# Kernel tuning notes

Measured on AMD Instinct MI355X. Metric: run time of the kernel, lower is better.

## Reference

```python
import jax, jax.numpy as jnp
import numpy as np

B, N, SD = 2, 128, 3
IN, H, BD, O, L, WF = 16, 128, 32, 12, 2, 4
DEGREE = 2
EPS = 1e-6


def fibonacci_lattice(n, offset=0.5):
    i = jnp.arange(n, dtype=jnp.float32)
    theta = (jnp.pi * i * (1.0 + np.sqrt(5.0))) % (2.0 * jnp.pi)
    phi = jnp.arccos(1.0 - 2.0 * (i + offset) / (n - 1 + 2 * offset))
    return jnp.stack((jnp.sin(phi) * jnp.cos(theta),
                      jnp.sin(phi) * jnp.sin(theta),
                      jnp.cos(phi)), axis=-1)  # (O, 3)


def poly_features(x, degree=DEGREE):
    feats = [x]
    for _ in range(degree):
        new = jnp.einsum('...i,...j->...ij', feats[-1], x).reshape(x.shape[:-1] + (-1,))
        feats.append(new)
    return jnp.concatenate(feats, axis=-1)


def layernorm(x, scale, bias):
    m = x.mean(axis=-1, keepdims=True)
    v = ((x - m) ** 2).mean(axis=-1, keepdims=True)
    return (x - m) * jax.lax.rsqrt(v + EPS) * scale + bias


def _dense(k, fin, fout):
    return jax.random.normal(k, (fin, fout), jnp.float32) / np.sqrt(fin)


def setup_inputs() -> dict:
    key = jax.random.key(0)
    ks = jax.random.split(key, 32)
    SP_IN = 2 + 4 + 8   # poly features of 2-dim spatial invariants, degree 2
    RO_IN = 1 + 1 + 1   # poly features of 1-dim orientation invariant
    inp = {
        'pos': jax.random.normal(ks[0], (B, N, SD), jnp.float32),
        'x': jax.random.normal(ks[1], (B, N, IN), jnp.float32),
        'mask': jnp.ones((B, N), jnp.float32),
        # spatial kernel basis MLP
        'W1s': _dense(ks[2], SP_IN, H), 'b1s': jnp.zeros((H,), jnp.float32),
        'W2s': _dense(ks[3], H, BD),    'b2s': jnp.zeros((BD,), jnp.float32),
        # rotation kernel basis MLP
        'W1r': _dense(ks[4], RO_IN, H), 'b1r': jnp.zeros((H,), jnp.float32),
        'W2r': _dense(ks[5], H, BD),    'b2r': jnp.zeros((BD,), jnp.float32),
        # x embedder (no bias)
        'We': _dense(ks[6], IN, H),
        # per-layer params, stacked along leading layer axis L
        'Wsp':  jax.random.normal(ks[7], (L, BD, H), jnp.float32) / np.sqrt(BD),
        'Wrot': jax.random.normal(ks[8], (L, BD, H), jnp.float32) / np.sqrt(BD),
        'conv_b': jnp.zeros((L, H), jnp.float32),
        'ln_scale': jnp.ones((L, H), jnp.float32),
        'ln_bias': jnp.zeros((L, H), jnp.float32),
        'Wl1': jax.random.normal(ks[9], (L, H, WF * H), jnp.float32) / np.sqrt(H),
        'bl1': jnp.zeros((L, WF * H), jnp.float32),
        'Wl2': jax.random.normal(ks[10], (L, WF * H, H), jnp.float32) / np.sqrt(WF * H),
        'bl2': jnp.zeros((L, H), jnp.float32),
        # readout
        'Wro': _dense(ks[11], H, 1), 'bro': jnp.zeros((1,), jnp.float32),
    }
    return inp


def reference(pos, x, mask, W1s, b1s, W2s, b2s, W1r, b1r, W2r, b2r, We,
              Wsp, Wrot, conv_b, ln_scale, ln_bias, Wl1, bl1, Wl2, bl2, Wro, bro):
    ori = fibonacci_lattice(O)                                   # (O, 3)
    # pairwise relative positions: (B, N_dst=m? note: original indexing)
    rel_pos = pos[:, None, :, None, :] - pos[:, :, None, None, :]  # (B,N,N,1,3)
    inv1 = (rel_pos * ori[None, None, None, :, :]).sum(-1, keepdims=True)        # (B,N,N,O,1)
    inv2 = jnp.linalg.norm(rel_pos - rel_pos * inv1, axis=-1, keepdims=True)     # (B,N,N,O,1)
    spatial_inv = jnp.concatenate([inv1, inv2], axis=-1)          # (B,N,N,O,2)
    ori_inv = (ori[:, None, :] * ori[None, :, :]).sum(-1, keepdims=True)         # (O,O,1)

    gelu = jax.nn.gelu  # approximate tanh gelu, matching flax nn.gelu default
    kernel_basis = gelu(gelu(poly_features(spatial_inv) @ W1s + b1s) @ W2s + b2s)   # (B,N,N,O,BD)
    fiber_basis = gelu(gelu(poly_features(ori_inv) @ W1r + b1r) @ W2r + b2r)        # (O,O,BD)

    h = x @ We                                                    # (B,N,H)
    h = jnp.broadcast_to(h[:, :, None, :], (h.shape[0], h.shape[1], O, h.shape[2]))

    for i in range(L):
        inp = h
        spatial_kernel = kernel_basis @ Wsp[i]                    # (B,N,N,O,H)
        rot_kernel = fiber_basis @ Wrot[i]                        # (O,O,H)
        h = jnp.einsum('bnoc,bmnoc,bn->bmoc', h, spatial_kernel, mask)
        h = jnp.einsum('bmoc,poc->bmpc', h, rot_kernel) / rot_kernel.shape[-2]
        h = h + conv_b[i]
        h = layernorm(h, ln_scale[i], ln_bias[i])
        h = gelu(h @ Wl1[i] + bl1[i]) @ Wl2[i] + bl2[i]
        h = h + inp

    readout = h @ Wro + bro                                       # (B,N,O,1)
    out_scalar = readout.mean(axis=-2)                            # (B,N,1)
    out_scalar = jnp.sum(out_scalar * mask[:, :, None], axis=1) / jnp.sum(mask[:, :, None], axis=1)
    return out_scalar                                             # (B,1)
```

## Files before the change

### kernel.cpp

```cpp
#include <hip/hip_runtime.h>
#include <math.h>

#define NB 2
#define NN 128
#define NO 12
#define NIN 16
#define NH 128
#define NBD 32
#define NL 2
#define NHH 512
#define NSPLIT 8

typedef __attribute__((ext_vector_type(8))) short bf16x8;
typedef __attribute__((ext_vector_type(4))) float f32x4;

__device__ __forceinline__ float gelu_f(float x){
    float x2 = x*x;
    float t = x*(2.3022077f + 0.1029435f*x2);
    float e = __builtin_amdgcn_exp2f(t);
    float r = __builtin_amdgcn_rcpf(e + 1.0f);
    return __builtin_fmaf(-x, r, x);
}

__device__ __forceinline__ ushort f2b(float x){
    union { float f; uint u; } v; v.f = x;
    uint r = v.u + 0x7FFF + ((v.u >> 16) & 1);
    return (ushort)(r >> 16);
}

#define MFMA_BF16(A,B,C) __builtin_amdgcn_mfma_f32_16x16x32_bf16(A,B,C,0,0,0)

__global__ __launch_bounds__(256) void k_setup(const float* __restrict__ W1r,
        const float* __restrict__ b1r, const float* __restrict__ W2r,
        const float* __restrict__ b2r, const float* __restrict__ W1s,
        const float* __restrict__ b1s, const float* __restrict__ W2s,
        float* __restrict__ ws_ori, float* __restrict__ ws_fiber,
        ushort* __restrict__ w1ct, ushort* __restrict__ w2ct){
    __shared__ float sori[NO*3];
    __shared__ float sb2r[NBD];
    __shared__ __align__(16) char sWT[8192];
    __shared__ __align__(16) char sHid[160*256];

    int tid = threadIdx.x;
    int w = tid >> 6, lane = tid & 63, lr = lane & 15, lg = lane >> 4;

    if (tid < NO){
        float fi = (float)tid;
        float th = fmodf(3.14159265358979323846f * fi * 3.23606797749979f,
                         6.28318530717958647692f);
        float ph = acosf(1.0f - 2.0f*(fi + 0.5f)/12.0f);
        float sp = sinf(ph);
        float ox = sp*cosf(th), oy = sp*sinf(th), oz = cosf(ph);
        sori[tid*3+0]=ox; sori[tid*3+1]=oy; sori[tid*3+2]=oz;
        ws_ori[tid*3+0]=ox; ws_ori[tid*3+1]=oy; ws_ori[tid*3+2]=oz;
    }
    if (tid < NBD) sb2r[tid] = b2r[tid];
    if (tid < NH){
        int c = tid;
        float r0 = b1s[c];
        float r1 = W1s[c], r2 = W1s[NH+c], r3 = W1s[2*NH+c];
        float r4 = W1s[3*NH+c] + W1s[4*NH+c];
        float r5 = W1s[5*NH+c], r6 = W1s[6*NH+c];
        float r7 = W1s[7*NH+c] + W1s[8*NH+c] + W1s[10*NH+c];
        float r8 = W1s[9*NH+c] + W1s[11*NH+c] + W1s[12*NH+c];
        float r9 = W1s[13*NH+c];
        ushort* p = w1ct + c*32;
        p[0]=f2b(r0); p[1]=f2b(r1); p[2]=f2b(r2); p[3]=f2b(r3); p[4]=f2b(r4);
        p[5]=f2b(r5); p[6]=f2b(r6); p[7]=f2b(r7); p[8]=f2b(r8); p[9]=f2b(r9);
        #pragma unroll
        for (int k = 10; k < 32; ++k) p[k] = 0;
    }
    for (int e = tid; e < NBD*NH; e += 256){
        int c = e >> 7, k = e & 127;
        w2ct[c*NH + k] = f2b(W2s[k*NBD + c]);
    }
    for (int e = tid; e < NBD*NH; e += 256){
        int c = e >> 7, k = e & 127;
        *(ushort*)(sWT + c*256 + ((k*2) ^ ((c & 7) << 4))) = f2b(W2r[k*NBD + c]);
    }
    for (int e = tid; e < 16*64; e += 256){
        int row = 144 + (e >> 6), k2 = e & 63;
        *(uint*)(sHid + row*256 + ((k2*4) ^ ((row & 7) << 4))) = 0u;
    }
    __syncthreads();
    for (int e = tid; e < 144*NH; e += 256){
        int t = e & 127, row = e >> 7;
        int p = row / NO, q = row - (row/NO)*NO;
        float xv = sori[p*3]*sori[q*3] + sori[p*3+1]*sori[q*3+1] + sori[p*3+2]*sori[q*3+2];
        float acc = b1r[t] + xv*(W1r[t] + xv*(W1r[NH+t] + xv*W1r[2*NH+t]));
        *(ushort*)(sHid + row*256 + ((t*2) ^ ((row & 7) << 4))) = f2b(gelu_f(acc));
    }
    __syncthreads();
    for (int tile = w; tile < 5; tile += 4){
        float bv0 = sb2r[lr], bv1 = sb2r[16 + lr];
        f32x4 acc2[2][2];
        acc2[0][0] = (f32x4){bv0,bv0,bv0,bv0}; acc2[0][1] = (f32x4){bv1,bv1,bv1,bv1};
        acc2[1][0] = acc2[0][0]; acc2[1][1] = acc2[0][1];
        #pragma unroll
        for (int kk = 0; kk < 4; ++kk){
            int kbyte = (kk*32 + lg*8)*2;
            int r0 = tile*32 + lr, r1 = r0 + 16;
            bf16x8 a0 = *(const bf16x8*)(sHid + r0*256 + (kbyte ^ ((r0 & 7) << 4)));
            bf16x8 a1 = *(const bf16x8*)(sHid + r1*256 + (kbyte ^ ((r1 & 7) << 4)));
            bf16x8 b0 = *(const bf16x8*)(sWT + lr*256 + (kbyte ^ ((lr & 7) << 4)));
            bf16x8 b1 = *(const bf16x8*)(sWT + (16+lr)*256 + (kbyte ^ ((lr & 7) << 4)));
            acc2[0][0] = MFMA_BF16(a0, b0, acc2[0][0]);
            acc2[0][1] = MFMA_BF16(a0, b1, acc2[0][1]);
            acc2[1][0] = MFMA_BF16(a1, b0, acc2[1][0]);
            acc2[1][1] = MFMA_BF16(a1, b1, acc2[1][1]);
        }
        #pragma unroll
        for (int i = 0; i < 2; ++i)
            #pragma unroll
            for (int j = 0; j < 2; ++j)
                #pragma unroll
                for (int r = 0; r < 4; ++r){
                    int row = tile*32 + i*16 + lg*4 + r, d = j*16 + lr;
                    if (row < 144) ws_fiber[row*NBD + d] = gelu_f(acc2[i][j][r]);
                }
    }
}

__global__ __launch_bounds__(256) void k_rot(const float* __restrict__ fiber,
        const float* __restrict__ Wrot, float* __restrict__ rot){
    int g = blockIdx.x*256 + threadIdx.x;
    int c = g & 127; int rest = g >> 7;
    int o = rest % NO; rest /= NO;
    int p = rest % NO; int i = rest / NO;
    const float* f = fiber + (p*NO + o)*NBD;
    const float* w = Wrot + (size_t)i*NBD*NH + c;
    float acc = 0.f;
    #pragma unroll
    for (int d = 0; d < NBD; ++d) acc += f[d]*w[d*NH];
    rot[g] = acc;
}

__global__ __launch_bounds__(256) void k_embed(const float* __restrict__ x,
        const float* __restrict__ We, float* __restrict__ hE){
    int g = blockIdx.x*256 + threadIdx.x;
    int c = g & 127; int n = (g >> 7) & 127; int b = g >> 14;
    const float* xp = x + ((size_t)b*NN + n)*NIN;
    float acc = 0.f;
    #pragma unroll
    for (int k = 0; k < NIN; ++k) acc += xp[k]*We[k*NH + c];
    hE[g] = acc;
}

__global__ __launch_bounds__(256) void k_kb(const float* __restrict__ pos,
        const ushort* __restrict__ w1ct, const ushort* __restrict__ w2ct,
        const float* __restrict__ b2s, const float* __restrict__ ori,
        ushort* __restrict__ kb){
    __shared__ __align__(16) char smem[49152];
    ushort* sF  = (ushort*)smem;
    char*  sWT  = smem + 8192;
    char*  sH   = smem + 16384;

    int tid = threadIdx.x;
    int bid = blockIdx.x;
    int m = bid & 127; int t2 = bid >> 7;
    int o = t2 % NO, b = t2 / NO;
    int w = tid >> 6, lane = tid & 63, lr = lane & 15, lg = lane >> 4;

    {
        const uint* src = (const uint*)w1ct;
        for (int e = tid; e < 2048; e += 256){
            int c = e >> 4, kk = e & 15;
            *(uint*)(sWT + c*64 + ((kk*4) ^ ((c & 3) << 4))) = src[e];
        }
    }
    if (tid < NN){
        int n = tid;
        float rx = pos[((size_t)b*NN+n)*3+0] - pos[((size_t)b*NN+m)*3+0];
        float ry = pos[((size_t)b*NN+n)*3+1] - pos[((size_t)b*NN+m)*3+1];
        float rz = pos[((size_t)b*NN+n)*3+2] - pos[((size_t)b*NN+m)*3+2];
        float ox = ori[o*3+0], oy = ori[o*3+1], oz = ori[o*3+2];
        float a  = rx*ox + ry*oy + rz*oz;
        float bb = sqrtf(rx*rx+ry*ry+rz*rz) * fabsf(1.0f - a);
        float a2 = a*a, b2 = bb*bb, ab = a*bb;
        float fv[10] = {1.0f, a, bb, a2, ab, b2, a2*a, a2*bb, a*b2, b2*bb};
        char* rowp = (char*)sF + n*64;
        int sw = (n & 3) << 4;
        #pragma unroll
        for (int kk = 0; kk < 5; ++kk){
            uint pk = (uint)f2b(fv[kk*2]) | ((uint)f2b(fv[kk*2+1]) << 16);
            *(uint*)(rowp + ((kk*4) ^ sw)) = pk;
        }
        #pragma unroll
        for (int kk = 5; kk < 16; ++kk)
            *(uint*)(rowp + ((kk*4) ^ sw)) = 0u;
    }
    __syncthreads();
    f32x4 hacc[2][8];
    {
        int rA0 = w*32 + lr, rA1 = rA0 + 16;
        bf16x8 fa0 = *(const bf16x8*)((char*)sF + rA0*64 + ((lg*16) ^ ((rA0 & 3) << 4)));
        bf16x8 fa1 = *(const bf16x8*)((char*)sF + rA1*64 + ((lg*16) ^ ((rA1 & 3) << 4)));
        #pragma unroll
        for (int j = 0; j < 8; ++j){
            int cB = j*16 + lr;
            bf16x8 fb = *(const bf16x8*)(sWT + cB*64 + ((lg*16) ^ ((cB & 3) << 4)));
            f32x4 z = (f32x4){0.f,0.f,0.f,0.f};
            hacc[0][j] = MFMA_BF16(fa0, fb, z);
            hacc[1][j] = MFMA_BF16(fa1, fb, z);
        }
    }
    #pragma unroll
    for (int i = 0; i < 2; ++i)
        #pragma unroll
        for (int j = 0; j < 8; ++j)
            #pragma unroll
            for (int r = 0; r < 4; ++r){
                int n = w*32 + i*16 + lg*4 + r;
                int c = j*16 + lr;
                *(ushort*)(sH + n*256 + ((c*2) ^ ((n & 7) << 4))) = f2b(gelu_f(hacc[i][j][r]));
            }
    __syncthreads();
    {
        const uint* src = (const uint*)w2ct;
        for (int e = tid; e < 2048; e += 256){
            int c = e >> 6, kk = e & 63;
            *(uint*)(sWT + c*256 + ((kk*4) ^ ((c & 7) << 4))) = src[e];
        }
    }
    __syncthreads();
    float bv0 = b2s[lr], bv1 = b2s[16 + lr];
    f32x4 acc2[2][2];
    acc2[0][0] = (f32x4){bv0,bv0,bv0,bv0}; acc2[0][1] = (f32x4){bv1,bv1,bv1,bv1};
    acc2[1][0] = acc2[0][0]; acc2[1][1] = acc2[0][1];
    #pragma unroll
    for (int kk = 0; kk < 4; ++kk){
        int kbyte = (kk*32 + lg*8)*2;
        int r0 = w*32 + lr, r1 = r0 + 16;
        bf16x8 a0 = *(const bf16x8*)(sH + r0*256 + (kbyte ^ ((r0 & 7) << 4)));
        bf16x8 a1 = *(const bf16x8*)(sH + r1*256 + (kbyte ^ ((r1 & 7) << 4)));
        bf16x8 b0 = *(const bf16x8*)(sWT + lr*256 + (kbyte ^ ((lr & 7) << 4)));
        bf16x8 b1 = *(const bf16x8*)(sWT + (16+lr)*256 + (kbyte ^ ((lr & 7) << 4)));
        acc2[0][0] = MFMA_BF16(a0, b0, acc2[0][0]);
        acc2[0][1] = MFMA_BF16(a0, b1, acc2[0][1]);
        acc2[1][0] = MFMA_BF16(a1, b0, acc2[1][0]);
        acc2[1][1] = MFMA_BF16(a1, b1, acc2[1][1]);
    }
    ushort* sOut = (ushort*)smem;
    #pragma unroll
    for (int i = 0; i < 2; ++i)
        #pragma unroll
        for (int j = 0; j < 2; ++j)
            #pragma unroll
            for (int r = 0; r < 4; ++r){
                int n = w*32 + i*16 + lg*4 + r, d = j*16 + lr;
                sOut[n*NBD + d] = f2b(gelu_f(acc2[i][j][r]));
            }
    __syncthreads();
    size_t base = ((size_t)((b*NO + o)*NN + m))*(NN*NBD);
    uint4* dst = (uint4*)(kb + base);
    const uint4* src = (const uint4*)sOut;
    dst[tid] = src[tid];
    dst[256 + tid] = src[256 + tid];
}

__global__ __launch_bounds__(256) void k_wbuild(const float* __restrict__ h,
        const float* __restrict__ wsp_i, const float* __restrict__ mask,
        ushort* __restrict__ Wt, int sB, int sP){
    __shared__ float sWspT[NH*33];
    __shared__ float sg[8*130];
    int tid = threadIdx.x;
    int bid = blockIdx.x;
    int ns = bid & 15; int rest = bid >> 4;
    int o = rest % NO, b = rest / NO;

    for (int e = tid; e < NBD*NH; e += 256){
        int c = e & 127, d = e >> 7;
        sWspT[c*33 + d] = wsp_i[d*NH + c];
    }
    for (int e = tid; e < 8*NH; e += 256){
        int n = e >> 7, c = e & 127;
        int ng = ns*8 + n;
        sg[n*130 + c] = h[(size_t)b*sB + (size_t)o*sP + (size_t)ng*NH + c] * mask[b*NN + ng];
    }
    __syncthreads();
    size_t obase = ((size_t)(b*NO + o)*NH)*(NN*NBD);
    #pragma unroll
    for (int it = 0; it < 16; ++it){
        int flat = it*256 + tid;
        int o8 = flat & 3, n = (flat >> 2) & 7, c = flat >> 5;
        float gv = sg[n*130 + c];
        ushort pk[8];
        #pragma unroll
        for (int dd = 0; dd < 8; ++dd)
            pk[dd] = f2b(gv * sWspT[c*33 + o8*8 + dd]);
        uint4 v;
        v.x = (uint)pk[0] | ((uint)pk[1] << 16);
        v.y = (uint)pk[2] | ((uint)pk[3] << 16);
        v.z = (uint)pk[4] | ((uint)pk[5] << 16);
        v.w = (uint)pk[6] | ((uint)pk[7] << 16);
        *(uint4*)(Wt + obase + (size_t)c*(NN*NBD) + (ns*8 + n)*NBD + o8*8) = v;
    }
}

__global__ __launch_bounds__(256) void k_convg(const ushort* __restrict__ kb,
        const ushort* __restrict__ Wt, float* __restrict__ part){
    __shared__ __align__(16) ushort sA[64*NH];
    __shared__ __align__(16) ushort sW[NH*NH];
    int tid = threadIdx.x;
    int bid = blockIdx.x;
    int s = bid & 7, mh = (bid >> 3) & 1;
    int rest = bid >> 4;
    int o = rest % NO, b = rest / NO;

    int w = tid >> 6, lane = tid & 63, lr = lane & 15, lg = lane >> 4;
    int wm = (w >> 1)*32, wc = (w & 1)*64;

    const ushort* abase = kb + ((size_t)(b*NO + o)*NN + mh*64)*(NN*NBD) + s*512;
    const ushort* wbase = Wt + ((size_t)(b*NO + o)*NH)*(NN*NBD) + s*512;

    f32x4 acc[2][4];
    #pragma unroll
    for (int i = 0; i < 2; ++i)
        #pragma unroll
        for (int j = 0; j < 4; ++j)
            acc[i][j] = (f32x4){0.f,0.f,0.f,0.f};

    for (int ch = 0; ch < 4; ++ch){
        #pragma unroll
        for (int it = 0; it < 4; ++it){
            int flat = it*256 + tid;
            int row = flat >> 4, seg = flat & 15;
            uint4 v = *(const uint4*)(abase + (size_t)row*(NN*NBD) + ch*128 + seg*8);
            *(uint4*)((char*)sA + row*256 + ((seg*16) ^ ((row & 7) << 4))) = v;
        }
        #pragma unroll
        for (int it = 0; it < 8; ++it){
            int flat = it*256 + tid;
            int row = flat >> 4, seg = flat & 15;
            uint4 v = *(const uint4*)(wbase + (size_t)row*(NN*NBD) + ch*128 + seg*8);
            *(uint4*)((char*)sW + row*256 + ((seg*16) ^ ((row & 7) << 4))) = v;
        }
        __syncthreads();
        #pragma unroll
        for (int kk = 0; kk < 4; ++kk){
            int kbyte = (kk*32 + lg*8)*2;
            int r0 = wm + lr, r1 = wm + 16 + lr;
            bf16x8 a0 = *(const bf16x8*)((const char*)sA + r0*256 + (kbyte ^ ((r0 & 7) << 4)));
            bf16x8 a1 = *(const bf16x8*)((const char*)sA + r1*256 + (kbyte ^ ((r1 & 7) << 4)));
            bf16x8 bf[4];
            #pragma unroll
            for (int j = 0; j < 4; ++j){
                int c = wc + j*16 + lr;
                bf[j] = *(const bf16x8*)((const char*)sW + c*256 + (kbyte ^ ((c & 7) << 4)));
            }
            #pragma unroll
            for (int j = 0; j < 4; ++j){
                acc[0][j] = MFMA_BF16(a0, bf[j], acc[0][j]);
                acc[1][j] = MFMA_BF16(a1, bf[j], acc[1][j]);
            }
        }
        __syncthreads();
    }
    float* pbase = part + ((size_t)((s*NB + b)*NO + o)*NN + mh*64)*NH;
    #pragma unroll
    for (int i = 0; i < 2; ++i)
        #pragma unroll
        for (int j = 0; j < 4; ++j)
            #pragma unroll
            for (int r = 0; r < 4; ++r){
                int mm = wm + i*16 + lg*4 + r;
                int c = wc + j*16 + lr;
                pbase[(size_t)mm*NH + c] = acc[i][j][r];
            }
}

__global__ __launch_bounds__(512) void k_mlp(const float* __restrict__ part,
        const float* __restrict__ hIn, float* __restrict__ hOut,
        const float* __restrict__ rot_i, const float* __restrict__ convb_i,
        const float* __restrict__ lns_i, const float* __restrict__ lnb_i,
        const float* __restrict__ Wl1_i, const float* __restrict__ bl1_i,
        const float* __restrict__ Wl2_i, const float* __restrict__ bl2_i,
        int sB, int sP){
    __shared__ float shcv[NO*NH];
    __shared__ float sy[NO*NH];
    __shared__ float sU[NO*NHH];
    __shared__ float sred[4*NO*NH];
    int tid = threadIdx.x;
    int bid = blockIdx.x;
    int m = bid & 127, b = bid >> 7;
    for (int e = tid; e < NO*NH; e += 512){
        int o = e >> 7, c = e & 127;
        float sv = 0.f;
        #pragma unroll
        for (int sl = 0; sl < NSPLIT; ++sl)
            sv += part[((size_t)((sl*NB + b)*NO + o)*NN + m)*NH + c];
        shcv[e] = sv;
    }
    __syncthreads();
    for (int e = tid; e < NO*NH; e += 512){
        int p = e >> 7, c = e & 127;
        float acc = 0.f;
        #pragma unroll
        for (int o = 0; o < NO; ++o)
            acc += shcv[o*NH + c]*rot_i[(p*NO + o)*NH + c];
        sy[e] = acc*(1.0f/12.0f) + convb_i[c];
    }
    __syncthreads();
    int wid = tid >> 6, lane = tid & 63;
    for (int row = wid; row < NO; row += 8){
        float x0 = sy[row*NH + lane], x1 = sy[row*NH + 64 + lane];
        float s = x0 + x1, ss = x0*x0 + x1*x1;
        for (int off = 32; off; off >>= 1){
            s  += __shfl_xor(s,  off);
            ss += __shfl_xor(ss, off);
        }
        float mn  = s*(1.0f/128.0f);
        float var = ss*(1.0f/128.0f) - mn*mn;
        float r = rsqrtf(var + 1e-6f);
        sy[row*NH + lane]      = (x0 - mn)*r*lns_i[lane]      + lnb_i[lane];
        sy[row*NH + 64 + lane] = (x1 - mn)*r*lns_i[64 + lane] + lnb_i[64 + lane];
    }
    __syncthreads();
    {
        int j = tid;
        float acc[NO];
        float bj = bl1_i[j];
        #pragma unroll
        for (int p = 0; p < NO; ++p) acc[p] = bj;
        for (int c0 = 0; c0 < NH; c0 += 4){
            f32x4 syv[NO];
            #pragma unroll
            for (int p = 0; p < NO; ++p) syv[p] = *(const f32x4*)&sy[p*NH + c0];
            #pragma unroll
            for (int cc = 0; cc < 4; ++cc){
                float wv = Wl1_i[(size_t)(c0+cc)*NHH + j];
                #pragma unroll
                for (int p = 0; p < NO; ++p) acc[p] += syv[p][cc]*wv;
            }
        }
        #pragma unroll
        for (int p = 0; p < NO; ++p) sU[p*NHH + j] = gelu_f(acc[p]);
    }
    __syncthreads();
    {
        int q = tid >> 7, c = tid & 127;
        float acc[NO];
        #pragma unroll
        for (int p = 0; p < NO; ++p) acc[p] = 0.f;
        for (int j0 = q*128; j0 < q*128 + 128; j0 += 4){
            f32x4 uv[NO];
            #pragma unroll
            for (int p = 0; p < NO; ++p) uv[p] = *(const f32x4*)&sU[p*NHH + j0];
            #pragma unroll
            for (int jj = 0; jj < 4; ++jj){
                float wv = Wl2_i[(size_t)(j0+jj)*NH + c];
                #pragma unroll
                for (int p = 0; p < NO; ++p) acc[p] += uv[p][jj]*wv;
            }
        }
        #pragma unroll
        for (int p = 0; p < NO; ++p) sred[(q*NO + p)*NH + c] = acc[p];
    }
    __syncthreads();
    for (int e = tid; e < NO*NH; e += 512){
        int p = e >> 7, c = e & 127;
        float v = sred[(0*NO+p)*NH + c] + sred[(1*NO+p)*NH + c]
                + sred[(2*NO+p)*NH + c] + sred[(3*NO+p)*NH + c];
        size_t gi = (((size_t)b*NO + p)*NN + m)*NH + c;
        size_t ri = (size_t)b*sB + (size_t)p*sP + (size_t)m*NH + c;
        hOut[gi] = v + bl2_i[c] + hIn[ri];
    }
}

__global__ __launch_bounds__(1024) void k_readout(const float* __restrict__ h,
        const float* __restrict__ Wro, const float* __restrict__ bro,
        const float* __restrict__ mask, float* __restrict__ out){
    __shared__ float sw[NH];
    __shared__ float sacc[16], smsk[16];
    int tid = threadIdx.x, b = blockIdx.x;
    if (tid < NH) sw[tid] = Wro[tid];
    __syncthreads();
    float br = bro[0];
    float acc = 0.f;
    for (int e = tid; e < NN*NO; e += 1024){
        int o = e % NO, mm = e / NO;
        const float4* hp = (const float4*)(h + (((size_t)b*NO + o)*NN + mm)*NH);
        const float4* swp = (const float4*)sw;
        float dot = 0.f;
        #pragma unroll
        for (int c = 0; c < NH/4; ++c){
            float4 hv = hp[c], wv = swp[c];
            dot += hv.x*wv.x + hv.y*wv.y + hv.z*wv.z + hv.w*wv.w;
        }
        acc += (dot + br)*mask[b*NN + mm];
    }
    float msum = (tid < NN) ? mask[b*NN + tid] : 0.f;
    for (int off = 32; off; off >>= 1){
        acc  += __shfl_xor(acc,  off);
        msum += __shfl_xor(msum, off);
    }
    if ((tid & 63) == 0){ sacc[tid>>6] = acc; smsk[tid>>6] = msum; }
    __syncthreads();
    if (tid == 0){
        float a = 0.f, mm2 = 0.f;
        #pragma unroll
        for (int i = 0; i < 16; ++i){ a += sacc[i]; mm2 += smsk[i]; }
        out[b] = a/(12.0f*mm2);
    }
}

extern "C" void kernel_launch(void* const* d_in, const int* in_sizes, int n_in,
                              void* d_out, int out_size, void* d_ws, size_t ws_size,
                              hipStream_t stream){
    const float* pos  = (const float*)d_in[0];
    const float* x    = (const float*)d_in[1];
    const float* mask = (const float*)d_in[2];
    const float* W1s  = (const float*)d_in[3];
    const float* b1s  = (const float*)d_in[4];
    const float* W2s  = (const float*)d_in[5];
    const float* b2s  = (const float*)d_in[6];
    const float* W1r  = (const float*)d_in[7];
    const float* b1r  = (const float*)d_in[8];
    const float* W2r  = (const float*)d_in[9];
    const float* b2r  = (const float*)d_in[10];
    const float* We   = (const float*)d_in[11];
    const float* Wsp  = (const float*)d_in[12];
    const float* Wrot = (const float*)d_in[13];
    const float* convb= (const float*)d_in[14];
    const float* lns  = (const float*)d_in[15];
    const float* lnb  = (const float*)d_in[16];
    const float* Wl1  = (const float*)d_in[17];
    const float* bl1  = (const float*)d_in[18];
    const float* Wl2  = (const float*)d_in[19];
    const float* bl2  = (const float*)d_in[20];
    const float* Wro  = (const float*)d_in[21];
    const float* bro  = (const float*)d_in[22];

    float* ws = (float*)d_ws;
    float* ws_ori = ws;
    float* ws_fib = ws + 64;
    float* ws_rot = ws + 64 + 4608;
    ushort* w1ct = (ushort*)(ws + 41536);
    ushort* w2ct = (ushort*)(ws + 43584);
    float* hE   = ws + 45632;
    float* hB   = hE + NB*NN*NH;
    float* hF   = hB + NB*NO*NN*NH;
    float* part = hF + NB*NO*NN*NH;
    ushort* kb  = (ushort*)(part + NSPLIT*NB*NO*NN*NH);
    ushort* Wt  = kb + (size_t)NB*NO*NN*NN*NBD;

    k_setup<<<1, 256, 0, stream>>>(W1r, b1r, W2r, b2r, W1s, b1s, W2s,
                                   ws_ori, ws_fib, w1ct, w2ct);
    k_rot<<<NL*NO*NO*NH/256, 256, 0, stream>>>(ws_fib, Wrot, ws_rot);
    k_embed<<<NB*NN*NH/256, 256, 0, stream>>>(x, We, hE);
    k_kb<<<NB*NO*NN, 256, 0, stream>>>(pos, w1ct, w2ct, b2s, ws_ori, kb);

    k_wbuild<<<NB*NO*16, 256, 0, stream>>>(hE, Wsp, mask, Wt, NN*NH, 0);
    k_convg<<<NB*NO*2*NSPLIT, 256, 0, stream>>>(kb, Wt, part);
    k_mlp<<<NB*NN, 512, 0, stream>>>(part, hE, hB,
            ws_rot, convb, lns, lnb,
            Wl1, bl1, Wl2, bl2, NN*NH, 0);
    k_wbuild<<<NB*NO*16, 256, 0, stream>>>(hB, Wsp + NBD*NH, mask, Wt,
            NO*NN*NH, NN*NH);
    k_convg<<<NB*NO*2*NSPLIT, 256, 0, stream>>>(kb, Wt, part);
    k_mlp<<<NB*NN, 512, 0, stream>>>(part, hB, hF,
            ws_rot + NO*NO*NH, convb + NH, lns + NH, lnb + NH,
            Wl1 + NH*NHH, bl1 + NHH, Wl2 + NHH*NH, bl2 + NH,
            NO*NN*NH, NN*NH);

    k_readout<<<NB, 1024, 0, stream>>>(hF, Wro, bro, mask, (float*)d_out);
}
```

Baseline: 278.5 us.

## Fuse weight build into conv GEMM, rot into setup, readout into MLP

The separate k_wbuild pass is removed: k_convg now builds each masked h*Wsp bf16 weight tile in shared memory on the fly, so the large Wt intermediate is never written to or read back from global memory. The k_rot kernel becomes an MFMA stage at the end of k_setup, and k_readout is folded into the final k_mlp through a per-row reduction and atomicAdd into a zeroed output. This cuts three launches and a large round trip through global memory, in exchange for extra conversion work inside the GEMM loop, higher register use for the Wsp column, and a run-to-run nondeterministic atomic summation order.

```diff
diff --git a/kernel.cpp b/kernel.cpp
--- a/kernel.cpp
+++ b/kernel.cpp
@@ -34,12 +34,16 @@
         const float* __restrict__ b1r, const float* __restrict__ W2r,
         const float* __restrict__ b2r, const float* __restrict__ W1s,
         const float* __restrict__ b1s, const float* __restrict__ W2s,
-        float* __restrict__ ws_ori, float* __restrict__ ws_fiber,
+        const float* __restrict__ Wrot, const float* __restrict__ mask,
+        float* __restrict__ ws_ori, float* __restrict__ ws_rot,
+        float* __restrict__ ws_rmask,
         ushort* __restrict__ w1ct, ushort* __restrict__ w2ct){
     __shared__ float sori[NO*3];
     __shared__ float sb2r[NBD];
     __shared__ __align__(16) char sWT[8192];
     __shared__ __align__(16) char sHid[160*256];
+    __shared__ __align__(16) char sFib[160*64];
+    __shared__ __align__(16) char sWrotT[2][8192];
 
     int tid = threadIdx.x;
     int w = tid >> 6, lane = tid & 63, lr = lane & 15, lg = lane >> 4;
@@ -55,6 +59,12 @@
         ws_ori[tid*3+0]=ox; ws_ori[tid*3+1]=oy; ws_ori[tid*3+2]=oz;
     }
     if (tid < NBD) sb2r[tid] = b2r[tid];
+    if (tid >= 32 && tid < 32 + NB){
+        int b = tid - 32;
+        float s = 0.f;
+        for (int mm = 0; mm < NN; ++mm) s += mask[b*NN + mm];
+        ws_rmask[b] = 1.0f/(12.0f*s);
+    }
     if (tid < NH){
         int c = tid;
         float r0 = b1s[c];
@@ -78,9 +88,19 @@
         int c = e >> 7, k = e & 127;
         *(ushort*)(sWT + c*256 + ((k*2) ^ ((c & 7) << 4))) = f2b(W2r[k*NBD + c]);
     }
+    for (int e = tid; e < 2*NH*16; e += 256){
+        int i = e >> 11, c = (e >> 4) & 127, kk = e & 15;
+        const float* wp = Wrot + (size_t)i*NBD*NH + c;
+        uint pk = (uint)f2b(wp[(size_t)(2*kk)*NH]) | ((uint)f2b(wp[(size_t)(2*kk+1)*NH]) << 16);
+        *(uint*)(sWrotT[i] + c*64 + ((kk*4) ^ ((c & 3) << 4))) = pk;
+    }
     for (int e = tid; e < 16*64; e += 256){
         int row = 144 + (e >> 6), k2 = e & 63;
         *(uint*)(sHid + row*256 + ((k2*4) ^ ((row & 7) << 4))) = 0u;
+    }
+    for (int e = tid; e < 16*16; e += 256){
+        int row = 144 + (e >> 4), k2 = e & 15;
+        *(uint*)(sFib + row*64 + ((k2*4) ^ ((row & 3) << 4))) = 0u;
     }
     __syncthreads();
     for (int e = tid; e < 144*NH; e += 256){
@@ -116,23 +136,30 @@
                 #pragma unroll
                 for (int r = 0; r < 4; ++r){
                     int row = tile*32 + i*16 + lg*4 + r, d = j*16 + lr;
-                    if (row < 144) ws_fiber[row*NBD + d] = gelu_f(acc2[i][j][r]);
+                    if (row < 144)
+                        *(ushort*)(sFib + row*64 + ((d*2) ^ ((row & 3) << 4)))
+                            = f2b(gelu_f(acc2[i][j][r]));
                 }
     }
-}
-
-__global__ __launch_bounds__(256) void k_rot(const float* __restrict__ fiber,
-        const float* __restrict__ Wrot, float* __restrict__ rot){
-    int g = blockIdx.x*256 + threadIdx.x;
-    int c = g & 127; int rest = g >> 7;
-    int o = rest % NO; rest /= NO;
-    int p = rest % NO; int i = rest / NO;
-    const float* f = fiber + (p*NO + o)*NBD;
-    const float* w = Wrot + (size_t)i*NBD*NH + c;
-    float acc = 0.f;
-    #pragma unroll
-    for (int d = 0; d < NBD; ++d) acc += f[d]*w[d*NH];
-    rot[g] = acc;
+    __syncthreads();
+    for (int job = w; job < 20; job += 4){
+        int i = job / 10, rt = job - (job/10)*10;
+        int rA = rt*16 + lr;
+        bf16x8 fa = *(const bf16x8*)(sFib + rA*64 + ((lg*16) ^ ((rA & 3) << 4)));
+        #pragma unroll
+        for (int j = 0; j < 8; ++j){
+            int cB = j*16 + lr;
+            bf16x8 fb = *(const bf16x8*)(sWrotT[i] + cB*64 + ((lg*16) ^ ((cB & 3) << 4)));
+            f32x4 z = (f32x4){0.f,0.f,0.f,0.f};
+            f32x4 acc = MFMA_BF16(fa, fb, z);
+            #pragma unroll
+            for (int r = 0; r < 4; ++r){
+                int row = rt*16 + lg*4 + r;
+                if (row < 144)
+                    ws_rot[(size_t)i*(144*NH) + (size_t)row*NH + j*16 + lr] = acc[r];
+            }
+        }
+    }
 }
 
 __global__ __launch_bounds__(256) void k_embed(const float* __restrict__ x,
@@ -258,47 +285,10 @@
     dst[256 + tid] = src[256 + tid];
 }
 
-__global__ __launch_bounds__(256) void k_wbuild(const float* __restrict__ h,
-        const float* __restrict__ wsp_i, const float* __restrict__ mask,
-        ushort* __restrict__ Wt, int sB, int sP){
-    __shared__ float sWspT[NH*33];
-    __shared__ float sg[8*130];
-    int tid = threadIdx.x;
-    int bid = blockIdx.x;
-    int ns = bid & 15; int rest = bid >> 4;
-    int o = rest % NO, b = rest / NO;
-
-    for (int e = tid; e < NBD*NH; e += 256){
-        int c = e & 127, d = e >> 7;
-        sWspT[c*33 + d] = wsp_i[d*NH + c];
-    }
-    for (int e = tid; e < 8*NH; e += 256){
-        int n = e >> 7, c = e & 127;
-        int ng = ns*8 + n;
-        sg[n*130 + c] = h[(size_t)b*sB + (size_t)o*sP + (size_t)ng*NH + c] * mask[b*NN + ng];
-    }
-    __syncthreads();
-    size_t obase = ((size_t)(b*NO + o)*NH)*(NN*NBD);
-    #pragma unroll
-    for (int it = 0; it < 16; ++it){
-        int flat = it*256 + tid;
-        int o8 = flat & 3, n = (flat >> 2) & 7, c = flat >> 5;
-        float gv = sg[n*130 + c];
-        ushort pk[8];
-        #pragma unroll
-        for (int dd = 0; dd < 8; ++dd)
-            pk[dd] = f2b(gv * sWspT[c*33 + o8*8 + dd]);
-        uint4 v;
-        v.x = (uint)pk[0] | ((uint)pk[1] << 16);
-        v.y = (uint)pk[2] | ((uint)pk[3] << 16);
-        v.z = (uint)pk[4] | ((uint)pk[5] << 16);
-        v.w = (uint)pk[6] | ((uint)pk[7] << 16);
-        *(uint4*)(Wt + obase + (size_t)c*(NN*NBD) + (ns*8 + n)*NBD + o8*8) = v;
-    }
-}
-
 __global__ __launch_bounds__(256) void k_convg(const ushort* __restrict__ kb,
-        const ushort* __restrict__ Wt, float* __restrict__ part){
+        const float* __restrict__ h, const float* __restrict__ wsp_i,
+        const float* __restrict__ mask, float* __restrict__ part,
+        int sB, int sP){
     __shared__ __align__(16) ushort sA[64*NH];
     __shared__ __align__(16) ushort sW[NH*NH];
     int tid = threadIdx.x;
@@ -310,8 +300,14 @@
     int w = tid >> 6, lane = tid & 63, lr = lane & 15, lg = lane >> 4;
     int wm = (w >> 1)*32, wc = (w & 1)*64;
 
+    int c_w = tid & 127, kh = tid >> 7;
+    float wv[NBD];
+    #pragma unroll
+    for (int d = 0; d < NBD; ++d) wv[d] = wsp_i[d*NH + c_w];
+
     const ushort* abase = kb + ((size_t)(b*NO + o)*NN + mh*64)*(NN*NBD) + s*512;
-    const ushort* wbase = Wt + ((size_t)(b*NO + o)*NH)*(NN*NBD) + s*512;
+    const float* hbase = h + (size_t)b*sB + (size_t)o*sP;
+    const float* mbase = mask + b*NN;
 
     f32x4 acc[2][4];
     #pragma unroll
@@ -329,11 +325,20 @@
             *(uint4*)((char*)sA + row*256 + ((seg*16) ^ ((row & 7) << 4))) = v;
         }
         #pragma unroll
-        for (int it = 0; it < 8; ++it){
-            int flat = it*256 + tid;
-            int row = flat >> 4, seg = flat & 15;
-            uint4 v = *(const uint4*)(wbase + (size_t)row*(NN*NBD) + ch*128 + seg*8);
-            *(uint4*)((char*)sW + row*256 + ((seg*16) ^ ((row & 7) << 4))) = v;
+        for (int u = 0; u < 2; ++u){
+            int n_loc = kh*2 + u;
+            int n = s*16 + ch*4 + n_loc;
+            float g = hbase[(size_t)n*NH + c_w] * mbase[n];
+            #pragma unroll
+            for (int q = 0; q < 4; ++q){
+                uint4 v;
+                v.x = (uint)f2b(g*wv[q*8+0]) | ((uint)f2b(g*wv[q*8+1]) << 16);
+                v.y = (uint)f2b(g*wv[q*8+2]) | ((uint)f2b(g*wv[q*8+3]) << 16);
+                v.z = (uint)f2b(g*wv[q*8+4]) | ((uint)f2b(g*wv[q*8+5]) << 16);
+                v.w = (uint)f2b(g*wv[q*8+6]) | ((uint)f2b(g*wv[q*8+7]) << 16);
+                int kbyte = (n_loc*32 + q*8)*2;
+                *(uint4*)((char*)sW + c_w*256 + (kbyte ^ ((c_w & 7) << 4))) = v;
+            }
         }
         __syncthreads();
         #pragma unroll
@@ -375,11 +380,14 @@
         const float* __restrict__ lns_i, const float* __restrict__ lnb_i,
         const float* __restrict__ Wl1_i, const float* __restrict__ bl1_i,
         const float* __restrict__ Wl2_i, const float* __restrict__ bl2_i,
-        int sB, int sP){
+        const float* __restrict__ Wro, const float* __restrict__ bro,
+        const float* __restrict__ mask, const float* __restrict__ rmask,
+        float* __restrict__ outp, int sB, int sP, int final){
     __shared__ float shcv[NO*NH];
     __shared__ float sy[NO*NH];
     __shared__ float sU[NO*NHH];
     __shared__ float sred[4*NO*NH];
+    __shared__ float swred[8];
     int tid = threadIdx.x;
     int bid = blockIdx.x;
     int m = bid & 127, b = bid >> 7;
@@ -457,50 +465,31 @@
         for (int p = 0; p < NO; ++p) sred[(q*NO + p)*NH + c] = acc[p];
     }
     __syncthreads();
+    float ro_part = 0.f;
     for (int e = tid; e < NO*NH; e += 512){
         int p = e >> 7, c = e & 127;
         float v = sred[(0*NO+p)*NH + c] + sred[(1*NO+p)*NH + c]
                 + sred[(2*NO+p)*NH + c] + sred[(3*NO+p)*NH + c];
-        size_t gi = (((size_t)b*NO + p)*NN + m)*NH + c;
         size_t ri = (size_t)b*sB + (size_t)p*sP + (size_t)m*NH + c;
-        hOut[gi] = v + bl2_i[c] + hIn[ri];
-    }
-}
-
-__global__ __launch_bounds__(1024) void k_readout(const float* __restrict__ h,
-        const float* __restrict__ Wro, const float* __restrict__ bro,
-        const float* __restrict__ mask, float* __restrict__ out){
-    __shared__ float sw[NH];
-    __shared__ float sacc[16], smsk[16];
-    int tid = threadIdx.x, b = blockIdx.x;
-    if (tid < NH) sw[tid] = Wro[tid];
-    __syncthreads();
-    float br = bro[0];
-    float acc = 0.f;
-    for (int e = tid; e < NN*NO; e += 1024){
-        int o = e % NO, mm = e / NO;
-        const float4* hp = (const float4*)(h + (((size_t)b*NO + o)*NN + mm)*NH);
-        const float4* swp = (const float4*)sw;
-        float dot = 0.f;
-        #pragma unroll
-        for (int c = 0; c < NH/4; ++c){
-            float4 hv = hp[c], wv = swp[c];
-            dot += hv.x*wv.x + hv.y*wv.y + hv.z*wv.z + hv.w*wv.w;
-        }
-        acc += (dot + br)*mask[b*NN + mm];
-    }
-    float msum = (tid < NN) ? mask[b*NN + tid] : 0.f;
-    for (int off = 32; off; off >>= 1){
-        acc  += __shfl_xor(acc,  off);
-        msum += __shfl_xor(msum, off);
-    }
-    if ((tid & 63) == 0){ sacc[tid>>6] = acc; smsk[tid>>6] = msum; }
-    __syncthreads();
-    if (tid == 0){
-        float a = 0.f, mm2 = 0.f;
-        #pragma unroll
-        for (int i = 0; i < 16; ++i){ a += sacc[i]; mm2 += smsk[i]; }
-        out[b] = a/(12.0f*mm2);
+        float vf = v + bl2_i[c] + hIn[ri];
+        if (!final){
+            size_t gi = (((size_t)b*NO + p)*NN + m)*NH + c;
+            hOut[gi] = vf;
+        } else {
+            ro_part += vf*Wro[c];
+        }
+    }
+    if (final){
+        for (int off = 32; off; off >>= 1) ro_part += __shfl_xor(ro_part, off);
+        if (lane == 0) swred[wid] = ro_part;
+        __syncthreads();
+        if (tid == 0){
+            float s = 0.f;
+            #pragma unroll
+            for (int i = 0; i < 8; ++i) s += swred[i];
+            float contrib = (s + 12.0f*bro[0]) * mask[b*NN + m] * rmask[b];
+            atomicAdd(&outp[b], contrib);
+        }
     }
 }
 
@@ -532,36 +521,33 @@
     const float* bro  = (const float*)d_in[22];
 
     float* ws = (float*)d_ws;
-    float* ws_ori = ws;
-    float* ws_fib = ws + 64;
-    float* ws_rot = ws + 64 + 4608;
-    ushort* w1ct = (ushort*)(ws + 41536);
-    ushort* w2ct = (ushort*)(ws + 43584);
-    float* hE   = ws + 45632;
+    float* ws_ori   = ws;
+    float* ws_rot   = ws + 64;
+    float* ws_rmask = ws + 64 + 36864;
+    ushort* w1ct = (ushort*)(ws + 36944);
+    ushort* w2ct = (ushort*)(ws + 38992);
+    float* hE   = ws + 41040;
     float* hB   = hE + NB*NN*NH;
-    float* hF   = hB + NB*NO*NN*NH;
-    float* part = hF + NB*NO*NN*NH;
+    float* part = hB + NB*NO*NN*NH;
     ushort* kb  = (ushort*)(part + NSPLIT*NB*NO*NN*NH);
-    ushort* Wt  = kb + (size_t)NB*NO*NN*NN*NBD;
+
+    hipMemsetAsync(d_out, 0, (size_t)out_size*sizeof(float), stream);
 
     k_setup<<<1, 256, 0, stream>>>(W1r, b1r, W2r, b2r, W1s, b1s, W2s,
-                                   ws_ori, ws_fib, w1ct, w2ct);
-    k_rot<<<NL*NO*NO*NH/256, 256, 0, stream>>>(ws_fib, Wrot, ws_rot);
+                                   Wrot, mask, ws_ori, ws_rot, ws_rmask,
+                                   w1ct, w2ct);
     k_embed<<<NB*NN*NH/256, 256, 0, stream>>>(x, We, hE);
     k_kb<<<NB*NO*NN, 256, 0, stream>>>(pos, w1ct, w2ct, b2s, ws_ori, kb);
 
-    k_wbuild<<<NB*NO*16, 256, 0, stream>>>(hE, Wsp, mask, Wt, NN*NH, 0);
-    k_convg<<<NB*NO*2*NSPLIT, 256, 0, stream>>>(kb, Wt, part);
+    k_convg<<<NB*NO*2*NSPLIT, 256, 0, stream>>>(kb, hE, Wsp, mask, part,
+            NN*NH, 0);
     k_mlp<<<NB*NN, 512, 0, stream>>>(part, hE, hB,
-            ws_rot, convb, lns, lnb,
-            Wl1, bl1, Wl2, bl2, NN*NH, 0);
-    k_wbuild<<<NB*NO*16, 256, 0, stream>>>(hB, Wsp + NBD*NH, mask, Wt,
+            ws_rot, convb, lns, lnb, Wl1, bl1, Wl2, bl2,
+            Wro, bro, mask, ws_rmask, (float*)d_out, NN*NH, 0, 0);
+    k_convg<<<NB*NO*2*NSPLIT, 256, 0, stream>>>(kb, hB, Wsp + NBD*NH, mask, part,
             NO*NN*NH, NN*NH);
-    k_convg<<<NB*NO*2*NSPLIT, 256, 0, stream>>>(kb, Wt, part);
-    k_mlp<<<NB*NN, 512, 0, stream>>>(part, hB, hF,
-            ws_rot + NO*NO*NH, convb + NH, lns + NH, lnb + NH,
+    k_mlp<<<NB*NN, 512, 0, stream>>>(part, hB, hB,
+            ws_rot + 144*NH, convb + NH, lns + NH, lnb + NH,
             Wl1 + NH*NHH, bl1 + NHH, Wl2 + NHH*NH, bl2 + NH,
-            NO*NN*NH, NN*NH);
-
-    k_readout<<<NB, 1024, 0, stream>>>(hF, Wro, bro, mask, (float*)d_out);
-}
+            Wro, bro, mask, ws_rmask, (float*)d_out, NO*NN*NH, NN*NH, 1);
+}
```

After: 261.2 us. 1.07x faster.
